# Kernel optimization log

Hardware: AMD Instinct MI355X
Metric: run time of the kernel (lower is better)

## Reference

```python
import jax, jax.numpy as jnp
import numpy as np

B, T, E, H = 16, 4096, 384, 64

def setup_inputs() -> dict:
    key = jax.random.key(0)
    k1, k2, k3, k4 = jax.random.split(key, 4)
    x = jax.random.normal(k1, (B, T, E), dtype=jnp.float32)
    # nn.Linear default init ~ U(-1/sqrt(fan_in), 1/sqrt(fan_in)); scale normals similarly
    s = 1.0 / np.sqrt(E)
    Wk = jax.random.uniform(k2, (E, H), dtype=jnp.float32, minval=-s, maxval=s)
    Wq = jax.random.uniform(k3, (E, H), dtype=jnp.float32, minval=-s, maxval=s)
    Wv = jax.random.uniform(k4, (E, H), dtype=jnp.float32, minval=-s, maxval=s)
    return {"x": x, "Wk": Wk, "Wq": Wq, "Wv": Wv}

def reference(x, Wk, Wq, Wv):
    b, t, c = x.shape
    k = x @ Wk          # [b,t,h]
    q = x @ Wq          # [b,t,h]
    v = x @ Wv          # [b,t,h]
    # scale by C**-0.5 where C is the embedding dim (as in source)
    scale = c ** (-0.5)
    weights = jnp.einsum('bqh,bkh->bqk', q, k) * scale  # [b,t,t]
    causal = jnp.tril(jnp.ones((t, t), dtype=bool))
    weights = jnp.where(causal, weights, -jnp.inf)
    weights = jax.nn.softmax(weights, axis=-1)
    # dropout is identity in eval mode
    out = jnp.einsum('bqk,bkh->bqh', weights, v)          # [b,t,h]
    return out
```

## Files before the change

### kernel.cpp

```cpp
#include <hip/hip_runtime.h>
#include <hip/hip_bf16.h>
#include <math.h>


typedef __attribute__((ext_vector_type(4))) float f32x4;
typedef __attribute__((ext_vector_type(8))) __bf16 bf16x8;

#define DEVI static __device__ __forceinline__

DEVI unsigned short f2bf(float f) {
  union { float f; unsigned int u; } x; x.f = f;
  unsigned int r = x.u + 0x7fffu + ((x.u >> 16) & 1u);
  return (unsigned short)(r >> 16);
}

DEVI unsigned int cvtpk_bf16(float lo, float hi) {
  unsigned int r;
  asm("v_cvt_pk_bf16_f32 %0, %1, %2" : "=v"(r) : "v"(lo), "v"(hi));
  return r;
}

DEVI f32x4 mfma16(bf16x8 a, bf16x8 b, f32x4 c) {
  return __builtin_amdgcn_mfma_f32_16x16x32_bf16(a, b, c, 0, 0, 0);
}

DEVI bf16x8 lds_frag(const unsigned short* buf, int row, int gran) {
  return *(const bf16x8*)(buf + row * 64 + ((gran ^ (row & 7)) << 3));
}

DEVI void gl_lds16(const unsigned short* g, unsigned short* l) {
  __builtin_amdgcn_global_load_lds(
      (const __attribute__((address_space(1))) unsigned int*)g,
      (__attribute__((address_space(3))) unsigned int*)l, 16, 0, 0);
}

__global__ __launch_bounds__(256) void k_pack(const float* __restrict__ Wk,
                                              const float* __restrict__ Wq,
                                              const float* __restrict__ Wv,
                                              unsigned short* __restrict__ WT) {
  int idx = blockIdx.x * 256 + threadIdx.x;
  if (idx >= 192 * 384) return;
  int n = idx / 384, k = idx - n * 384;
  const float* W = (n < 64) ? Wk : ((n < 128) ? Wq : Wv);
  float val = W[k * 64 + (n & 63)];
  if (n >= 64 && n < 128) val *= 0.073622223f;
  WT[idx] = f2bf(val);
}

__global__ __launch_bounds__(256, 4) void k_proj(const float* __restrict__ x,
                                                 const unsigned short* __restrict__ WT,
                                                 unsigned short* __restrict__ Y,
                                                 unsigned short* __restrict__ VT) {
  __shared__ __align__(16) unsigned short As[64 * 64];
  __shared__ __align__(16) unsigned short Bs[192 * 64];
  const int tid = threadIdx.x;
  const int lane = tid & 63, wid = tid >> 6;
  const int q = lane & 15, g = lane >> 4;
  const int wm = wid >> 1, wn = wid & 1;
  const int m0 = blockIdx.x * 64;

  f32x4 acc[2][6];
#pragma unroll
  for (int mt = 0; mt < 2; ++mt)
#pragma unroll
    for (int nt = 0; nt < 6; ++nt) acc[mt][nt] = f32x4{0.f, 0.f, 0.f, 0.f};

  const int ar = tid >> 2, ap = tid & 3;

  for (int ks = 0; ks < 6; ++ks) {
    const float4* xp = (const float4*)(x + (size_t)(m0 + ar) * 384 + ks * 64 + ap * 16);
#pragma unroll
    for (int cc = 0; cc < 2; ++cc) {
      float4 f0 = xp[cc * 2], f1 = xp[cc * 2 + 1];
      union { unsigned short h[8]; uint4 v; } u;
      u.h[0] = f2bf(f0.x); u.h[1] = f2bf(f0.y); u.h[2] = f2bf(f0.z); u.h[3] = f2bf(f0.w);
      u.h[4] = f2bf(f1.x); u.h[5] = f2bf(f1.y); u.h[6] = f2bf(f1.z); u.h[7] = f2bf(f1.w);
      int gran = ap * 2 + cc;
      *(uint4*)(As + ar * 64 + ((gran ^ (ar & 7)) << 3)) = u.v;
    }
#pragma unroll
    for (int i = 0; i < 6; ++i) {
      int c = tid + 256 * i;
      int row = c >> 3, gr = c & 7;
      uint4 w = *(const uint4*)(WT + (size_t)row * 384 + ks * 64 + gr * 8);
      *(uint4*)(Bs + row * 64 + ((gr ^ (row & 7)) << 3)) = w;
    }
    __syncthreads();
#pragma unroll
    for (int kk = 0; kk < 2; ++kk) {
      bf16x8 af[2], bfv[6];
#pragma unroll
      for (int mt = 0; mt < 2; ++mt) af[mt] = lds_frag(As, wm * 32 + mt * 16 + q, kk * 4 + g);
#pragma unroll
      for (int nt = 0; nt < 6; ++nt) bfv[nt] = lds_frag(Bs, wn * 96 + nt * 16 + q, kk * 4 + g);
#pragma unroll
      for (int mt = 0; mt < 2; ++mt)
#pragma unroll
        for (int nt = 0; nt < 6; ++nt) acc[mt][nt] = mfma16(af[mt], bfv[nt], acc[mt][nt]);
    }
    __syncthreads();
  }
#pragma unroll
  for (int mt = 0; mt < 2; ++mt) {
    const int mrow = m0 + wm * 32 + mt * 16 + g * 4;
#pragma unroll
    for (int nt = 0; nt < 6; ++nt) {
      const int ncol = wn * 96 + nt * 16 + q;
      if (wn == 1 && nt >= 2) {
        const int d = (nt - 2) * 16 + q;
        const int bb = mrow >> 12, t = mrow & 4095;
        uint2 pv;
        pv.x = cvtpk_bf16(acc[mt][nt][0], acc[mt][nt][1]);
        pv.y = cvtpk_bf16(acc[mt][nt][2], acc[mt][nt][3]);
        *(uint2*)(VT + (size_t)(bb * 64 + d) * 4096 + t) = pv;
      } else {
        size_t base = (size_t)mrow * 128 + ncol;
#pragma unroll
        for (int j = 0; j < 4; ++j) Y[base + (size_t)j * 128] = f2bf(acc[mt][nt][j]);
      }
    }
  }
}

__global__ __launch_bounds__(512, 4) void k_attn(const unsigned short* __restrict__ Y,
                                                 const unsigned short* __restrict__ VT,
                                                 float* __restrict__ out) {
  __shared__ __align__(16) unsigned short Ks[4][64 * 64];
  __shared__ __align__(16) unsigned short Vs[4][64 * 64];

  const int id = blockIdx.x;
  const int xcd = id & 7;
  const int b = xcd * 2 + ((id >> 3) & 1);
  const int rank = id >> 4;
  const int i = (rank < 16) ? (31 - rank) : (rank - 16);
  const int q0 = i * 128;
  const int nkv = 2 * i + 2;

  const int tid = threadIdx.x;
  const int lane = tid & 63, wid = tid >> 6;
  const int p = wid >> 2;
  const int w4 = wid & 3;
  const int q = lane & 15, g = lane >> 4;

  const unsigned short* Yb = Y + (size_t)b * 4096 * 128;
  const unsigned short* Vb = VT + (size_t)b * 64 * 4096;

#define STAGE(S, KV0)                                                           \
  {                                                                             \
    int r = tid >> 3, grs = (tid & 7) ^ (r & 7);                                \
    int kp = (r & 32) | ((r & 12) << 1) | ((r & 16) >> 2) | (r & 3);            \
    gl_lds16(Yb + (size_t)((KV0) + kp) * 128 + grs * 8, Ks[S] + tid * 8);       \
    gl_lds16(Vb + (size_t)r * 4096 + (KV0) + grs * 8, Vs[S] + tid * 8);         \
  }

  STAGE(0, 0)
  STAGE(1, 64)
  __syncthreads();

  bf16x8 qf[2][2];
#pragma unroll
  for (int qh = 0; qh < 2; ++qh) {
    const unsigned short* qp = Yb + (size_t)(q0 + w4 * 32 + qh * 16 + q) * 128 + 64;
    qf[qh][0] = *(const bf16x8*)(qp + g * 8);
    qf[qh][1] = *(const bf16x8*)(qp + 32 + g * 8);
  }

  f32x4 accO[2][4];
#pragma unroll
  for (int qh = 0; qh < 2; ++qh)
#pragma unroll
    for (int dt = 0; dt < 4; ++dt) accO[qh][dt] = f32x4{0.f, 0.f, 0.f, 0.f};
  float lsum[2] = {0.f, 0.f};

  const int mytiles = 2 * i + 1 + (w4 >> 1);
  const int nIt = nkv >> 1;

  for (int it = 0; it < nIt; ++it) {
    const int kt = 2 * it + p;
    const int t2 = 2 * it + 2, t3 = 2 * it + 3;
    if (t2 < nkv) STAGE(t2 & 3, t2 * 64)
    if (t3 < nkv) STAGE(t3 & 3, t3 * 64)

    if (kt < mytiles) {
      const int kv0 = kt * 64;
      const unsigned short* Kc = Ks[kt & 3];
      const unsigned short* Vc = Vs[kt & 3];

      bf16x8 ka0[4], ka1[4];
#pragma unroll
      for (int t = 0; t < 4; ++t) {
        ka0[t] = lds_frag(Kc, t * 16 + q, g);
        ka1[t] = lds_frag(Kc, t * 16 + q, 4 + g);
      }
      f32x4 accS[2][4];
      __builtin_amdgcn_s_setprio(1);
#pragma unroll
      for (int qh = 0; qh < 2; ++qh)
#pragma unroll
        for (int t = 0; t < 4; ++t) {
          f32x4 z = f32x4{0.f, 0.f, 0.f, 0.f};
          z = mfma16(ka0[t], qf[qh][0], z);
          z = mfma16(ka1[t], qf[qh][1], z);
          accS[qh][t] = z;
        }
      __builtin_amdgcn_s_setprio(0);

      const bool dmw = (kv0 + 63 >= q0 + w4 * 32);
      bf16x8 bp[2][2];
#pragma unroll
      for (int qh = 0; qh < 2; ++qh) {
        if (dmw) {
          const int qrow = q0 + w4 * 32 + qh * 16 + q;
#pragma unroll
          for (int t = 0; t < 4; ++t)
#pragma unroll
            for (int j = 0; j < 4; ++j) {
              const int kvl = ((t >> 1) << 5) + (g << 3) + ((t & 1) << 2) + j;
              if (kv0 + kvl > qrow) accS[qh][t][j] = -INFINITY;
            }
        }
        float pp[4][4];
        float ps0 = 0.f, ps1 = 0.f;
#pragma unroll
        for (int t = 0; t < 4; ++t) {
          pp[t][0] = __builtin_amdgcn_exp2f(accS[qh][t][0]);
          pp[t][1] = __builtin_amdgcn_exp2f(accS[qh][t][1]);
          pp[t][2] = __builtin_amdgcn_exp2f(accS[qh][t][2]);
          pp[t][3] = __builtin_amdgcn_exp2f(accS[qh][t][3]);
          ps0 += pp[t][0] + pp[t][1];
          ps1 += pp[t][2] + pp[t][3];
        }
        lsum[qh] += ps0 + ps1;
        uint4 u0, u1;
        u0.x = cvtpk_bf16(pp[0][0], pp[0][1]);
        u0.y = cvtpk_bf16(pp[0][2], pp[0][3]);
        u0.z = cvtpk_bf16(pp[1][0], pp[1][1]);
        u0.w = cvtpk_bf16(pp[1][2], pp[1][3]);
        u1.x = cvtpk_bf16(pp[2][0], pp[2][1]);
        u1.y = cvtpk_bf16(pp[2][2], pp[2][3]);
        u1.z = cvtpk_bf16(pp[3][0], pp[3][1]);
        u1.w = cvtpk_bf16(pp[3][2], pp[3][3]);
        bp[qh][0] = __builtin_bit_cast(bf16x8, u0);
        bp[qh][1] = __builtin_bit_cast(bf16x8, u1);
      }

      __builtin_amdgcn_s_setprio(1);
#pragma unroll
      for (int dt = 0; dt < 4; ++dt) {
        bf16x8 av0 = lds_frag(Vc, dt * 16 + q, g);
        bf16x8 av1 = lds_frag(Vc, dt * 16 + q, 4 + g);
#pragma unroll
        for (int qh = 0; qh < 2; ++qh) {
          accO[qh][dt] = mfma16(av0, bp[qh][0], accO[qh][dt]);
          accO[qh][dt] = mfma16(av1, bp[qh][1], accO[qh][dt]);
        }
      }
      __builtin_amdgcn_s_setprio(0);
    }

    __syncthreads();
  }
#undef STAGE

#pragma unroll
  for (int qh = 0; qh < 2; ++qh) {
    lsum[qh] += __shfl_xor(lsum[qh], 16);
    lsum[qh] += __shfl_xor(lsum[qh], 32);
  }

  float* scrO = (float*)Ks;
  float* scrL = (float*)Vs;
  const int si = (w4 * 64 + lane) * 2;
  if (p == 1) {
#pragma unroll
    for (int qh = 0; qh < 2; ++qh) {
      float* so = scrO + (si + qh) * 16;
#pragma unroll
      for (int dt = 0; dt < 4; ++dt) *(float4*)(so + dt * 4) = *(float4*)&accO[qh][dt];
      scrL[si + qh] = lsum[qh];
    }
  }
  __syncthreads();
  if (p == 0) {
#pragma unroll
    for (int qh = 0; qh < 2; ++qh) {
      const float* so = scrO + (si + qh) * 16;
      float rl = 1.0f / (lsum[qh] + scrL[si + qh]);
      const int qrow = q0 + w4 * 32 + qh * 16 + q;
      float* op = out + (size_t)(b * 4096 + qrow) * 64;
#pragma unroll
      for (int dt = 0; dt < 4; ++dt) {
        float4 ob = *(const float4*)(so + dt * 4);
        f32x4 vO;
        vO[0] = (accO[qh][dt][0] + ob.x) * rl;
        vO[1] = (accO[qh][dt][1] + ob.y) * rl;
        vO[2] = (accO[qh][dt][2] + ob.z) * rl;
        vO[3] = (accO[qh][dt][3] + ob.w) * rl;
        *(float4*)(op + dt * 16 + g * 4) = *(float4*)&vO;
      }
    }
  }
}

extern "C" void kernel_launch(void* const* d_in, const int* in_sizes, int n_in,
                              void* d_out, int out_size, void* d_ws, size_t ws_size,
                              hipStream_t stream) {
  const float* x  = (const float*)d_in[0];
  const float* Wk = (const float*)d_in[1];
  const float* Wq = (const float*)d_in[2];
  const float* Wv = (const float*)d_in[3];
  float* out = (float*)d_out;

  unsigned short* WT = (unsigned short*)d_ws;
  unsigned short* Y  = WT + 73728;
  unsigned short* VT = Y + 8388608;

  hipLaunchKernelGGL(k_pack, dim3(288), dim3(256), 0, stream, Wk, Wq, Wv, WT);
  hipLaunchKernelGGL(k_proj, dim3(1024), dim3(256), 0, stream, x, WT, Y, VT);
  hipLaunchKernelGGL(k_attn, dim3(512), dim3(512), 0, stream, Y, VT, out);
}
```

Before: 86.57 us.

## Split long causal query blocks across two workgroups with a reduction pass

The 16 longest query blocks per batch are each split into two halves of the KV range, processed by separate workgroups that write unnormalized bf16 partial outputs and row sums to workspace. A new reduction kernel adds the halves and normalizes into the output. The grid grows from 512 to 768 blocks so the causal workload is balanced and the tail shortens. The cost is an extra kernel launch, extra global traffic for the partials, and bf16 rounding of the intermediate accumulators, which is safe only because the running max is not tracked per half.

```diff
diff --git a/kernel.cpp b/kernel.cpp
--- a/kernel.cpp
+++ b/kernel.cpp
@@ -12,6 +12,11 @@
   union { float f; unsigned int u; } x; x.f = f;
   unsigned int r = x.u + 0x7fffu + ((x.u >> 16) & 1u);
   return (unsigned short)(r >> 16);
+}
+
+DEVI float bf2f(unsigned int u) {
+  union { unsigned int u; float f; } x; x.u = u << 16;
+  return x.f;
 }
 
 DEVI unsigned int cvtpk_bf16(float lo, float hi) {
@@ -124,17 +129,34 @@
 
 __global__ __launch_bounds__(512, 4) void k_attn(const unsigned short* __restrict__ Y,
                                                  const unsigned short* __restrict__ VT,
-                                                 float* __restrict__ out) {
+                                                 float* __restrict__ out,
+                                                 unsigned short* __restrict__ PO,
+                                                 float* __restrict__ PL) {
   __shared__ __align__(16) unsigned short Ks[4][64 * 64];
   __shared__ __align__(16) unsigned short Vs[4][64 * 64];
 
   const int id = blockIdx.x;
   const int xcd = id & 7;
   const int b = xcd * 2 + ((id >> 3) & 1);
-  const int rank = id >> 4;
-  const int i = (rank < 16) ? (31 - rank) : (rank - 16);
+  const int idx = id >> 4;
+  int i, itBeg, itEnd, h;
+  bool split;
+  if (idx < 32) {
+    split = true;
+    i = 16 + (idx >> 1);
+    h = idx & 1;
+    const int nIt = i + 1, nH0 = (nIt + 1) >> 1;
+    itBeg = h ? nH0 : 0;
+    itEnd = h ? nIt : nH0;
+  } else {
+    split = false;
+    i = 47 - idx;
+    h = 0;
+    itBeg = 0;
+    itEnd = i + 1;
+  }
   const int q0 = i * 128;
-  const int nkv = 2 * i + 2;
+  const int tEnd = 2 * itEnd;
 
   const int tid = threadIdx.x;
   const int lane = tid & 63, wid = tid >> 6;
@@ -153,8 +175,11 @@
     gl_lds16(Vb + (size_t)r * 4096 + (KV0) + grs * 8, Vs[S] + tid * 8);         \
   }
 
-  STAGE(0, 0)
-  STAGE(1, 64)
+  {
+    const int tb = 2 * itBeg;
+    STAGE(tb & 3, tb * 64)
+    STAGE((tb + 1) & 3, (tb + 1) * 64)
+  }
   __syncthreads();
 
   bf16x8 qf[2][2];
@@ -173,13 +198,12 @@
   float lsum[2] = {0.f, 0.f};
 
   const int mytiles = 2 * i + 1 + (w4 >> 1);
-  const int nIt = nkv >> 1;
-
-  for (int it = 0; it < nIt; ++it) {
+
+  for (int it = itBeg; it < itEnd; ++it) {
     const int kt = 2 * it + p;
     const int t2 = 2 * it + 2, t3 = 2 * it + 3;
-    if (t2 < nkv) STAGE(t2 & 3, t2 * 64)
-    if (t3 < nkv) STAGE(t3 & 3, t3 * 64)
+    if (t2 < tEnd) STAGE(t2 & 3, t2 * 64)
+    if (t3 < tEnd) STAGE(t3 & 3, t3 * 64)
 
     if (kt < mytiles) {
       const int kv0 = kt * 64;
@@ -282,24 +306,67 @@
   }
   __syncthreads();
   if (p == 0) {
-#pragma unroll
-    for (int qh = 0; qh < 2; ++qh) {
-      const float* so = scrO + (si + qh) * 16;
-      float rl = 1.0f / (lsum[qh] + scrL[si + qh]);
-      const int qrow = q0 + w4 * 32 + qh * 16 + q;
-      float* op = out + (size_t)(b * 4096 + qrow) * 64;
-#pragma unroll
-      for (int dt = 0; dt < 4; ++dt) {
-        float4 ob = *(const float4*)(so + dt * 4);
-        f32x4 vO;
-        vO[0] = (accO[qh][dt][0] + ob.x) * rl;
-        vO[1] = (accO[qh][dt][1] + ob.y) * rl;
-        vO[2] = (accO[qh][dt][2] + ob.z) * rl;
-        vO[3] = (accO[qh][dt][3] + ob.w) * rl;
-        *(float4*)(op + dt * 16 + g * 4) = *(float4*)&vO;
-      }
-    }
-  }
+    if (!split) {
+#pragma unroll
+      for (int qh = 0; qh < 2; ++qh) {
+        const float* so = scrO + (si + qh) * 16;
+        float rl = 1.0f / (lsum[qh] + scrL[si + qh]);
+        const int qrow = q0 + w4 * 32 + qh * 16 + q;
+        float* op = out + (size_t)(b * 4096 + qrow) * 64;
+#pragma unroll
+        for (int dt = 0; dt < 4; ++dt) {
+          float4 ob = *(const float4*)(so + dt * 4);
+          f32x4 vO;
+          vO[0] = (accO[qh][dt][0] + ob.x) * rl;
+          vO[1] = (accO[qh][dt][1] + ob.y) * rl;
+          vO[2] = (accO[qh][dt][2] + ob.z) * rl;
+          vO[3] = (accO[qh][dt][3] + ob.w) * rl;
+          *(float4*)(op + dt * 16 + g * 4) = *(float4*)&vO;
+        }
+      }
+    } else {
+      const int jobj = (b << 4) + (i - 16);
+      unsigned short* PO_ = PO + ((size_t)(jobj * 2 + h)) * 8192;
+      float* PL_ = PL + (jobj * 2 + h) * 128;
+#pragma unroll
+      for (int qh = 0; qh < 2; ++qh) {
+        const float* so = scrO + (si + qh) * 16;
+        const float lt = lsum[qh] + scrL[si + qh];
+        const int row = w4 * 32 + qh * 16 + q;
+        if (g == 0) PL_[row] = lt;
+#pragma unroll
+        for (int dt = 0; dt < 4; ++dt) {
+          float4 ob = *(const float4*)(so + dt * 4);
+          uint2 pv;
+          pv.x = cvtpk_bf16(accO[qh][dt][0] + ob.x, accO[qh][dt][1] + ob.y);
+          pv.y = cvtpk_bf16(accO[qh][dt][2] + ob.z, accO[qh][dt][3] + ob.w);
+          *(uint2*)(PO_ + row * 64 + dt * 16 + g * 4) = pv;
+        }
+      }
+    }
+  }
+}
+
+__global__ __launch_bounds__(256) void k_red(const unsigned short* __restrict__ PO,
+                                             const float* __restrict__ PL,
+                                             float* __restrict__ out) {
+  const int idx = blockIdx.x * 256 + threadIdx.x;
+  const int dq = idx & 15;
+  const int row = (idx >> 4) & 127;
+  const int j = idx >> 11;
+  const int b = j >> 4, i = 16 + (j & 15);
+
+  const unsigned short* a0 = PO + ((size_t)(j * 2)) * 8192 + row * 64 + dq * 4;
+  const uint2 u0 = *(const uint2*)a0;
+  const uint2 u1 = *(const uint2*)(a0 + 8192);
+  const float rl = 1.0f / (PL[(j * 2) * 128 + row] + PL[(j * 2 + 1) * 128 + row]);
+
+  float4 o;
+  o.x = (bf2f(u0.x & 0xffffu) + bf2f(u1.x & 0xffffu)) * rl;
+  o.y = (bf2f(u0.x >> 16) + bf2f(u1.x >> 16)) * rl;
+  o.z = (bf2f(u0.y & 0xffffu) + bf2f(u1.y & 0xffffu)) * rl;
+  o.w = (bf2f(u0.y >> 16) + bf2f(u1.y >> 16)) * rl;
+  *(float4*)(out + ((size_t)(b * 4096 + i * 128 + row)) * 64 + dq * 4) = o;
 }
 
 extern "C" void kernel_launch(void* const* d_in, const int* in_sizes, int n_in,
@@ -314,8 +381,11 @@
   unsigned short* WT = (unsigned short*)d_ws;
   unsigned short* Y  = WT + 73728;
   unsigned short* VT = Y + 8388608;
+  unsigned short* PO = VT + 4194304;
+  float*          PL = (float*)(PO + 4194304);
 
   hipLaunchKernelGGL(k_pack, dim3(288), dim3(256), 0, stream, Wk, Wq, Wv, WT);
   hipLaunchKernelGGL(k_proj, dim3(1024), dim3(256), 0, stream, x, WT, Y, VT);
-  hipLaunchKernelGGL(k_attn, dim3(512), dim3(512), 0, stream, Y, VT, out);
-}
+  hipLaunchKernelGGL(k_attn, dim3(768), dim3(512), 0, stream, Y, VT, out, PO, PL);
+  hipLaunchKernelGGL(k_red, dim3(2048), dim3(256), 0, stream, PO, PL, out);
+}
```

New measurement: 85.90 us. No clear change (-0.8%).
